# Optimization experiments

Measured on AMD Instinct MI355X. Metric: run time of the kernel, lower is better.

Reference implementation:

```python
import jax, jax.numpy as jnp
import numpy as np

B, T, H, NIN, D = 128, 64, 100, 3, 10


def _gru_cell(x, h, Wih, Whh, bih, bhh):
    # torch GRU cell: r,z,n gate ordering
    gi = x @ Wih.T + bih
    gh = h @ Whh.T + bhh
    ir, iz, inn = jnp.split(gi, 3, axis=-1)
    hr, hz, hn = jnp.split(gh, 3, axis=-1)
    r = jax.nn.sigmoid(ir + hr)
    z = jax.nn.sigmoid(iz + hz)
    n = jnp.tanh(inn + r * hn)
    return (1.0 - z) * n + z * h


def setup_inputs():
    keys = iter(jax.random.split(jax.random.key(0), 64))
    def rn(shape, scale):
        return jax.random.normal(next(keys), shape, dtype=jnp.float32) * scale
    inp = {"received": jax.random.normal(next(keys), (B, T, NIN), dtype=jnp.float32)}
    s = float(1.0 / np.sqrt(H))
    for p in ("w1", "w2"):
        inp[p + "_ih0"] = rn((3 * H, NIN), s)
        inp[p + "_hh0"] = rn((3 * H, H), s)
        inp[p + "_bih0"] = rn((3 * H,), s)
        inp[p + "_bhh0"] = rn((3 * H,), s)
        inp[p + "_ih1"] = rn((3 * H, H), s)
        inp[p + "_hh1"] = rn((3 * H, H), s)
        inp[p + "_bih1"] = rn((3 * H,), s)
        inp[p + "_bhh1"] = rn((3 * H,), s)
    s2 = float(1.0 / np.sqrt(2 * H))
    inp["attn_w"] = rn((1, 2 * H), s2)
    inp["attn_b"] = rn((1,), s2)
    inp["ctx_w"] = rn((H, 2 * H), s2)
    inp["ctx_b"] = rn((H,), s2)
    inp["out_w"] = rn((1, 2 * H), s2)
    inp["out_b"] = rn((1,), s2)
    return inp


def _forward(received, P1, P2, attn_w, attn_b, ctx_w, ctx_b, out_w, out_b):
    def two_layer(x, h, P):
        ih0, hh0, bih0, bhh0, ih1, hh1, bih1, bhh1 = P
        h0 = _gru_cell(x, h[0], ih0, hh0, bih0, bhh0)
        h1 = _gru_cell(h0, h[1], ih1, hh1, bih1, bhh1)
        # out = top-layer hidden; new hidden state [2,B,H]
        return h1, jnp.stack([h0, h1])

    def attend(hn, cache, t):
        # hn [2,B,H] (raw GRU hidden), cache [2,B,T,H] of past raw hiddens
        hrep = jnp.broadcast_to(hn[:, :, None, :], cache.shape)
        e = (jnp.concatenate([hrep, cache], axis=-1) @ attn_w.T)[..., 0] + attn_b[0]  # [2,B,T]
        mask = jnp.arange(T) < jnp.maximum(t, 1)  # safe mask (never all-False)
        a = jax.nn.softmax(jnp.where(mask, e, -1e30), axis=-1)
        c = jnp.einsum('lbt,lbth->lbh', a, cache)
        return jnp.concatenate([c, hn], axis=-1) @ ctx_w.T + ctx_b

    x_tm = jnp.transpose(received, (1, 0, 2))  # [T,B,NIN]
    h_init = jnp.zeros((2, B, H), jnp.float32)
    cache_init = jnp.zeros((2, B, T, H), jnp.float32)

    def step(carry, inp):
        h1, h2, c1, c2 = carry
        x, t = inp
        o1, h1n = two_layer(x, h1, P1)
        o2, h2n = two_layer(x, h2, P2)
        # attention over hiddens from steps 0..t-1 (cache updated AFTER attending)
        h1mix = attend(h1n, c1, t)
        h2mix = attend(h2n, c2, t)
        c1 = jax.lax.dynamic_update_slice(c1, h1n[:, :, None, :], (0, 0, t, 0))
        c2 = jax.lax.dynamic_update_slice(c2, h2n[:, :, None, :], (0, 0, t, 0))
        first = (t == 0)
        h1next = jnp.where(first, h1n, h1mix)
        h2next = jnp.where(first, h2n, h2mix)
        return (h1next, h2next, c1, c2), (o1, o2)

    _, (out1, out2) = jax.lax.scan(step, (h_init, h_init, cache_init, cache_init),
                                   (x_tm, jnp.arange(T)))
    out1 = jnp.transpose(out1, (1, 0, 2))  # [B,T,H]
    out2 = jnp.transpose(out2, (1, 0, 2))
    # readout: bit i pairs rnn_out1[i] with rnn_out2[min(i+D, T-1)]
    idx = jnp.minimum(jnp.arange(T) + D, T - 1)
    rnn_out = jnp.concatenate([out1, out2[:, idx, :]], axis=-1)  # [B,T,2H]
    logits = rnn_out @ out_w.T + out_b  # dec_act == 'linear'
    return jax.nn.sigmoid(logits)  # [B,T,1]


def reference(received, w1_ih0, w1_hh0, w1_bih0, w1_bhh0, w1_ih1, w1_hh1, w1_bih1, w1_bhh1,
              w2_ih0, w2_hh0, w2_bih0, w2_bhh0, w2_ih1, w2_hh1, w2_bih1, w2_bhh1,
              attn_w, attn_b, ctx_w, ctx_b, out_w, out_b):
    P1 = (w1_ih0, w1_hh0, w1_bih0, w1_bhh0, w1_ih1, w1_hh1, w1_bih1, w1_bhh1)
    P2 = (w2_ih0, w2_hh0, w2_bih0, w2_bhh0, w2_ih1, w2_hh1, w2_bih1, w2_bhh1)
    return _forward(received, P1, P2, attn_w, attn_b, ctx_w, ctx_b, out_w, out_b)
```

## Files before the change

### kernel.cpp

```cpp
#include <hip/hip_runtime.h>
#include <stdint.h>

#define H100 100
#define T64  64
#define NB   128
#define DLAG 10

#define OFF_HH0 0
#define OFF_IH1 30000
#define OFF_HH1 60000
#define OFF_CTX 90000
#define OFF_AWC 100000
#define OFF_OW  100050
#define OFF_P   100152

typedef _Float16 half2_t __attribute__((ext_vector_type(2)));
typedef __fp16   pk16x2  __attribute__((ext_vector_type(2)));

__device__ __forceinline__ float fdot2u(uint32_t a, uint32_t b, float c) {
#if __has_builtin(__builtin_amdgcn_fdot2)
    return __builtin_amdgcn_fdot2(__builtin_bit_cast(half2_t, a),
                                  __builtin_bit_cast(half2_t, b), c, false);
#else
    half2_t ha = __builtin_bit_cast(half2_t, a), hb = __builtin_bit_cast(half2_t, b);
    return c + (float)ha[0]*(float)hb[0] + (float)ha[1]*(float)hb[1];
#endif
}
__device__ __forceinline__ uint32_t pkrtz(float a, float b) {
    pk16x2 h = __builtin_amdgcn_cvt_pkrtz(a, b);
    return __builtin_bit_cast(uint32_t, h);
}
__device__ __forceinline__ uint32_t pk_rn(float a, float b) {
    half2_t h; h[0] = (_Float16)a; h[1] = (_Float16)b;
    return __builtin_bit_cast(uint32_t, h);
}
__device__ __forceinline__ float lo16(uint32_t u){ return (float)__builtin_bit_cast(half2_t,u)[0]; }
__device__ __forceinline__ float hi16(uint32_t u){ return (float)__builtin_bit_cast(half2_t,u)[1]; }
__device__ __forceinline__ float sigm(float x){ return 1.f/(1.f+__expf(-x)); }
__device__ __forceinline__ float tanhfast(float x){ return 1.f - 2.f/(1.f+__expf(2.f*x)); }
__device__ __forceinline__ float gru_el(float pr, float pz, float gin, float ghn, float hp) {
    float r = sigm(pr), z = sigm(pz);
    float n = tanhfast(gin + r*ghn);
    return (1.f - z)*n + z*hp;
}
__device__ __forceinline__ float wsum(float v){
    #pragma unroll
    for (int off = 32; off; off >>= 1) v += __shfl_xor(v, off);
    return v;
}
__device__ __forceinline__ float wmax(float v){
    #pragma unroll
    for (int off = 32; off; off >>= 1) v = fmaxf(v, __shfl_xor(v, off));
    return v;
}

struct SMem {
    alignas(16) uint32_t cache_t[2][50][66];
    alignas(16) float grz1[200];
    alignas(16) float gin1[104];
    alignas(16) float ghn1[104];
    alignas(16) float grz2[200];
    alignas(16) float gin2[104];
    alignas(16) float ghn2[104];
    alignas(16) float sv[2][64];
    alignas(16) float atile[2][64];
    alignas(16) uint32_t cpkq[2][52];
    alignas(16) uint32_t h0c[52];
    alignas(16) uint32_t h1c[52];
    alignas(16) uint32_t hn0[52];
    alignas(16) uint32_t hn1[52];
    alignas(16) float x[192];
};

__global__ void prep_pack(const float* __restrict__ w1hh0, const float* __restrict__ w2hh0,
                          const float* __restrict__ w1ih1, const float* __restrict__ w2ih1,
                          const float* __restrict__ w1hh1, const float* __restrict__ w2hh1,
                          const float* __restrict__ attw,  const float* __restrict__ ctxw,
                          const float* __restrict__ outw,  uint32_t* __restrict__ ws) {
    int g = blockIdx.x*blockDim.x + threadIdx.x;
    if (g < 30000) {
        int br = g/15000, idx = g%15000;
        int j = idx/50, kp = idx%50;
        const float* w = br ? w2hh0 : w1hh0;
        ws[OFF_HH0 + g] = pk_rn(w[j*H100+2*kp], w[j*H100+2*kp+1]);
    } else if (g < 60000) {
        int t2 = g-30000; int br = t2/15000, idx = t2%15000;
        int j = idx/50, kp = idx%50;
        const float* w = br ? w2ih1 : w1ih1;
        ws[OFF_IH1 + t2] = pk_rn(w[j*H100+2*kp], w[j*H100+2*kp+1]);
    } else if (g < 90000) {
        int t2 = g-60000; int br = t2/15000, idx = t2%15000;
        int j = idx/50, kp = idx%50;
        const float* w = br ? w2hh1 : w1hh1;
        ws[OFF_HH1 + t2] = pk_rn(w[j*H100+2*kp], w[j*H100+2*kp+1]);
    } else if (g < 100000) {
        int idx = g-90000; int o = idx/100, kp = idx%100;
        ws[OFF_CTX + idx] = pk_rn(ctxw[o*200+2*kp], ctxw[o*200+2*kp+1]);
    } else if (g < 100050) {
        int i2 = g-100000;
        ws[OFF_AWC + i2] = pk_rn(attw[100+2*i2], attw[101+2*i2]);
    } else if (g < 100150) {
        int t2 = g-100050; int br = t2/50, i2 = t2%50;
        ws[OFF_OW + t2] = pk_rn(outw[br*H100+2*i2], outw[br*H100+2*i2+1]);
    }
}

__global__ __launch_bounds__(512, 1)
void gru_seq(const float* __restrict__ recv,
             const float* __restrict__ ih0_1, const float* __restrict__ bih0_1,
             const float* __restrict__ bhh0_1, const float* __restrict__ bih1_1,
             const float* __restrict__ bhh1_1,
             const float* __restrict__ ih0_2, const float* __restrict__ bih0_2,
             const float* __restrict__ bhh0_2, const float* __restrict__ bih1_2,
             const float* __restrict__ bhh1_2,
             const float* __restrict__ ctxb,
             uint32_t* __restrict__ ws) {
    __shared__ SMem S;
    const int tid = threadIdx.x;
    const int w   = tid >> 6;
    const int la  = tid & 63;
    const int br  = blockIdx.x >> 7;
    const int b   = blockIdx.x & 127;

    const float* ih0 = br ? ih0_2  : ih0_1;
    const float* bi0 = br ? bih0_2 : bih0_1;
    const float* bh0 = br ? bhh0_2 : bhh0_1;
    const float* bi1 = br ? bih1_2 : bih1_1;
    const float* bh1 = br ? bhh1_2 : bhh1_1;

    for (int i = tid; i < 192; i += 512) S.x[i] = recv[b*192 + i];
    for (int i = tid; i < 2*50*66; i += 512) ((uint32_t*)S.cache_t)[i] = 0u;
    if (tid < 128) S.sv[tid>>6][tid&63] = 0.f;
    if (tid < 104) { S.cpkq[0][tid>>1] = 0u; S.cpkq[1][tid>>1] = 0u; }
    if (tid >= 128 && tid < 180) { int i2 = tid-128; S.h0c[i2]=0u; S.h1c[i2]=0u; S.hn0[i2]=0u; S.hn1[i2]=0u; }

    uint32_t wreg[150];
    float fb0=0.f, fb1=0.f, fb2=0.f, fb3=0.f;
    float rix0=0.f, rix1=0.f, rix2=0.f;
    int cl=0, co=0;
    if (tid < 300) {
        const uint32_t* p0 = ws + OFF_HH0 + br*15000 + tid*50;
        const uint32_t* p1 = ws + OFF_HH1 + br*15000 + tid*50;
        const uint32_t* p2 = ws + OFF_IH1 + br*15000 + tid*50;
        #pragma unroll
        for (int k = 0; k < 50; ++k) { wreg[k] = p0[k]; wreg[50+k] = p1[k]; wreg[100+k] = p2[k]; }
        fb0 = bi0[tid]; fb1 = bh0[tid]; fb2 = bi1[tid]; fb3 = bh1[tid];
        rix0 = ih0[tid*3]; rix1 = ih0[tid*3+1]; rix2 = ih0[tid*3+2];
    } else if (tid < 500) {
        const int idx = tid - 300;
        cl = (idx >= 100) ? 1 : 0;
        co = idx - cl*100;
        const uint32_t* pc = ws + OFF_CTX + co*100;
        #pragma unroll
        for (int k = 0; k < 100; ++k) wreg[k] = pc[k];
        fb0 = ctxb[co];
    }
    uint32_t rawc = 0u, rowp = 0u;
    if ((w == 5 || w == 6) && la < 50) rawc = ws[OFF_AWC + la];
    if (w == 7 && la < 50) rowp = ws[OFF_OW + br*50 + la];
    float* p_out = (float*)(ws + OFF_P);

    float gh1save = 0.f;
    __syncthreads();

    for (int t = 0; t < T64; ++t) {
        if (tid < 300) {
            float x0 = S.x[3*t], x1 = S.x[3*t+1], x2 = S.x[3*t+2];
            float accI = fb0 + rix0*x0 + rix1*x1 + rix2*x2;
            float a0=0.f,a1=0.f,a2=0.f,a3=0.f, b0=0.f,b1=0.f,b2=0.f,b3=0.f;
            #pragma unroll
            for (int i = 0; i < 12; ++i) {
                uint4 h0 = *(const uint4*)&S.h0c[4*i];
                uint4 h1 = *(const uint4*)&S.h1c[4*i];
                a0 = fdot2u(wreg[4*i],    h0.x, a0);
                b0 = fdot2u(wreg[50+4*i], h1.x, b0);
                a1 = fdot2u(wreg[4*i+1],    h0.y, a1);
                b1 = fdot2u(wreg[50+4*i+1], h1.y, b1);
                a2 = fdot2u(wreg[4*i+2],    h0.z, a2);
                b2 = fdot2u(wreg[50+4*i+2], h1.z, b2);
                a3 = fdot2u(wreg[4*i+3],    h0.w, a3);
                b3 = fdot2u(wreg[50+4*i+3], h1.w, b3);
            }
            {
                uint2 h0t = *(const uint2*)&S.h0c[48];
                uint2 h1t = *(const uint2*)&S.h1c[48];
                a0 = fdot2u(wreg[48],    h0t.x, a0);
                b0 = fdot2u(wreg[98],    h1t.x, b0);
                a1 = fdot2u(wreg[49],    h0t.y, a1);
                b1 = fdot2u(wreg[99],    h1t.y, b1);
            }
            float acc0 = fb1 + ((a0+a1)+(a2+a3));
            gh1save    = fb3 + ((b0+b1)+(b2+b3));
            if (tid < 200) S.grz1[tid] = accI + acc0;
            else { S.gin1[tid-200] = accI; S.ghn1[tid-200] = acc0; }
        } else if (w == 5 || w == 6) {
            const int l = w - 5;
            const int m = (t > 1) ? t : 1;
            float sval = S.sv[l][la];
            float sv2  = (la < m) ? sval : -3e38f;
            float mx   = wmax(sv2);
            float p    = (la < m) ? __expf(sv2 - mx) : 0.f;
            float ssum = wsum(p);
            S.atile[l][la] = p;
            if (la < 50) {
                float c0 = 0.f, c1 = 0.f;
                const uint32_t* crow = &S.cache_t[l][la][0];
                const int np = (m + 1) >> 1;
                for (int tb = 0; tb < np; tb += 8) {
                    float2 ap[8]; uint2 cp[8];
                    #pragma unroll
                    for (int j = 0; j < 8; ++j) {
                        ap[j] = *(const float2*)&S.atile[l][2*(tb+j)];
                        cp[j] = *(const uint2*)&crow[2*(tb+j)];
                    }
                    #pragma unroll
                    for (int j = 0; j < 8; ++j) {
                        c0 += ap[j].x*lo16(cp[j].x) + ap[j].y*lo16(cp[j].y);
                        c1 += ap[j].x*hi16(cp[j].x) + ap[j].y*hi16(cp[j].y);
                    }
                }
                float inv = 1.f/ssum;
                S.cpkq[l][la] = pkrtz(c0*inv, c1*inv);
            }
        }
        __syncthreads();
        if (w == 5) {
            uint32_t hn0p = 0u;
            if (la < 50) {
                float2 pr = *(const float2*)&S.grz1[2*la];
                float2 pz = *(const float2*)&S.grz1[100+2*la];
                float2 gi = *(const float2*)&S.gin1[2*la];
                float2 gh = *(const float2*)&S.ghn1[2*la];
                uint32_t hp = S.h0c[la];
                float h0 = gru_el(pr.x, pz.x, gi.x, gh.x, lo16(hp));
                float h1 = gru_el(pr.y, pz.y, gi.y, gh.y, hi16(hp));
                hn0p = pkrtz(h0, h1);
                S.hn0[la] = hn0p;
                S.cache_t[0][la][t] = hn0p;
            }
            float v = (la < 50) ? fdot2u(rawc, hn0p, 0.f) : 0.f;
            v = wsum(v);
            if (la == 0) S.sv[0][t] = v;
        } else if (w == 7 && t > 0) {
            float v = (la < 50) ? fdot2u(rowp, S.hn1[la], 0.f) : 0.f;
            v = wsum(v);
            if (la == 0) p_out[br*8192 + b*64 + (t-1)] = v;
        }
        __syncthreads();
        if (tid < 300) {
            float g0=0.f,g1=0.f,g2=0.f,g3=0.f;
            #pragma unroll
            for (int i = 0; i < 12; ++i) {
                uint4 h = *(const uint4*)&S.hn0[4*i];
                g0 = fdot2u(wreg[100+4*i],   h.x, g0);
                g1 = fdot2u(wreg[100+4*i+1], h.y, g1);
                g2 = fdot2u(wreg[100+4*i+2], h.z, g2);
                g3 = fdot2u(wreg[100+4*i+3], h.w, g3);
            }
            {
                uint2 ht = *(const uint2*)&S.hn0[48];
                g0 = fdot2u(wreg[148], ht.x, g0);
                g1 = fdot2u(wreg[149], ht.y, g1);
            }
            float gi1 = fb2 + ((g0+g1)+(g2+g3));
            if (tid < 200) S.grz2[tid] = gi1 + gh1save;
            else { S.gin2[tid-200] = gi1; S.ghn2[tid-200] = gh1save; }
        }
        __syncthreads();
        if (w == 6) {
            uint32_t hn1p = 0u;
            if (la < 50) {
                float2 pr = *(const float2*)&S.grz2[2*la];
                float2 pz = *(const float2*)&S.grz2[100+2*la];
                float2 gi = *(const float2*)&S.gin2[2*la];
                float2 gh = *(const float2*)&S.ghn2[2*la];
                uint32_t hp = S.h1c[la];
                float h0 = gru_el(pr.x, pz.x, gi.x, gh.x, lo16(hp));
                float h1 = gru_el(pr.y, pz.y, gi.y, gh.y, hi16(hp));
                hn1p = pkrtz(h0, h1);
                S.hn1[la] = hn1p;
                S.cache_t[1][la][t] = hn1p;
            }
            float v = (la < 50) ? fdot2u(rawc, hn1p, 0.f) : 0.f;
            v = wsum(v);
            if (la == 0) S.sv[1][t] = v;
        }
        __syncthreads();
        if (tid >= 300 && tid < 500) {
            const uint32_t* cparr = S.cpkq[cl];
            const uint32_t* hnarr = cl ? S.hn1 : S.hn0;
            float p0=fb0, p1=0.f, p2=0.f, p3=0.f;
            float q0=0.f, q1=0.f, q2=0.f, q3=0.f;
            #pragma unroll
            for (int i = 0; i < 12; ++i) {
                uint4 c = *(const uint4*)&cparr[4*i];
                uint4 h = *(const uint4*)&hnarr[4*i];
                p0 = fdot2u(wreg[4*i],   c.x, p0);
                q0 = fdot2u(wreg[50+4*i],   h.x, q0);
                p1 = fdot2u(wreg[4*i+1], c.y, p1);
                q1 = fdot2u(wreg[50+4*i+1], h.y, q1);
                p2 = fdot2u(wreg[4*i+2], c.z, p2);
                q2 = fdot2u(wreg[50+4*i+2], h.z, q2);
                p3 = fdot2u(wreg[4*i+3], c.w, p3);
                q3 = fdot2u(wreg[50+4*i+3], h.w, q3);
            }
            {
                uint2 c = *(const uint2*)&cparr[48];
                uint2 h = *(const uint2*)&hnarr[48];
                p0 = fdot2u(wreg[48], c.x, p0);
                q0 = fdot2u(wreg[98], h.x, q0);
                p1 = fdot2u(wreg[49], c.y, p1);
                q1 = fdot2u(wreg[99], h.y, q1);
            }
            float m0 = ((p0+p1)+(p2+p3)) + ((q0+q1)+(q2+q3));
            float n0 = __shfl_down(m0, 1);
            if (!(co & 1)) {
                uint32_t packed = (t == 0) ? hnarr[co>>1] : pkrtz(m0, n0);
                if (cl) S.h1c[co>>1] = packed; else S.h0c[co>>1] = packed;
            }
        }
        __syncthreads();
    }
    if (w == 7) {
        float v = (la < 50) ? fdot2u(rowp, S.hn1[la], 0.f) : 0.f;
        v = wsum(v);
        if (la == 0) p_out[br*8192 + b*64 + 63] = v;
    }
}

__global__ void fin_out(const uint32_t* __restrict__ ws, const float* __restrict__ outb,
                        float* __restrict__ out) {
    int i = blockIdx.x*blockDim.x + threadIdx.x;
    if (i >= NB*T64) return;
    int b = i >> 6, t = i & 63;
    const float* p = (const float*)(ws + OFF_P);
    int t2 = t + DLAG; if (t2 > T64-1) t2 = T64-1;
    float logit = p[0*8192 + b*64 + t] + p[1*8192 + b*64 + t2] + outb[0];
    out[i] = 1.f/(1.f+__expf(-logit));
}

extern "C" void kernel_launch(void* const* d_in, const int* in_sizes, int n_in,
                              void* d_out, int out_size, void* d_ws, size_t ws_size,
                              hipStream_t stream) {
    const float* recv   = (const float*)d_in[0];
    const float* w1ih0  = (const float*)d_in[1];
    const float* w1hh0  = (const float*)d_in[2];
    const float* w1bih0 = (const float*)d_in[3];
    const float* w1bhh0 = (const float*)d_in[4];
    const float* w1ih1  = (const float*)d_in[5];
    const float* w1hh1  = (const float*)d_in[6];
    const float* w1bih1 = (const float*)d_in[7];
    const float* w1bhh1 = (const float*)d_in[8];
    const float* w2ih0  = (const float*)d_in[9];
    const float* w2hh0  = (const float*)d_in[10];
    const float* w2bih0 = (const float*)d_in[11];
    const float* w2bhh0 = (const float*)d_in[12];
    const float* w2ih1  = (const float*)d_in[13];
    const float* w2hh1  = (const float*)d_in[14];
    const float* w2bih1 = (const float*)d_in[15];
    const float* w2bhh1 = (const float*)d_in[16];
    const float* attw   = (const float*)d_in[17];
    const float* ctxw   = (const float*)d_in[19];
    const float* ctxb   = (const float*)d_in[20];
    const float* outw   = (const float*)d_in[21];
    const float* outb   = (const float*)d_in[22];
    uint32_t* ws = (uint32_t*)d_ws;
    float* out = (float*)d_out;

    prep_pack<<<(100150 + 255)/256, 256, 0, stream>>>(
        w1hh0, w2hh0, w1ih1, w2ih1, w1hh1, w2hh1, attw, ctxw, outw, ws);

    gru_seq<<<256, 512, 0, stream>>>(
        recv,
        w1ih0, w1bih0, w1bhh0, w1bih1, w1bhh1,
        w2ih0, w2bih0, w2bhh0, w2bih1, w2bhh1,
        ctxb, ws);

    fin_out<<<(NB*T64 + 255)/256, 256, 0, stream>>>(ws, outb, out);
}
```

Measured before the change: 227.1 us.

## Split ctx matvec across 400 threads and move layer-1 hh matvec to phase two

The context projection is now split in half along K across 400 threads (tid 100..499), each holding 50 packed weights in a separate register array; the halves are combined with a lane shuffle. The layer-1 recurrent matvec (h1c · W_hh1) moves from the first phase into the second phase, which otherwise only runs the small GRU elementwise warps. The aim is to shorten the critical path of phases one and three so the serial per-timestep barrier chain gets shorter. The cost is extra registers in threads that hold both wreg and creg (tid 100..299), which may hurt occupancy or cause spills.

```diff
diff --git a/kernel.cpp b/kernel.cpp
--- a/kernel.cpp
+++ b/kernel.cpp
@@ -135,9 +135,10 @@
     if (tid >= 128 && tid < 180) { int i2 = tid-128; S.h0c[i2]=0u; S.h1c[i2]=0u; S.hn0[i2]=0u; S.hn1[i2]=0u; }
 
     uint32_t wreg[150];
-    float fb0=0.f, fb1=0.f, fb2=0.f, fb3=0.f;
+    uint32_t creg[50];
+    float fb0=0.f, fb1=0.f, fb2=0.f, fb3=0.f, fcb=0.f;
     float rix0=0.f, rix1=0.f, rix2=0.f;
-    int cl=0, co=0;
+    int kh=0, cl=0, co=0;
     if (tid < 300) {
         const uint32_t* p0 = ws + OFF_HH0 + br*15000 + tid*50;
         const uint32_t* p1 = ws + OFF_HH1 + br*15000 + tid*50;
@@ -146,14 +147,16 @@
         for (int k = 0; k < 50; ++k) { wreg[k] = p0[k]; wreg[50+k] = p1[k]; wreg[100+k] = p2[k]; }
         fb0 = bi0[tid]; fb1 = bh0[tid]; fb2 = bi1[tid]; fb3 = bh1[tid];
         rix0 = ih0[tid*3]; rix1 = ih0[tid*3+1]; rix2 = ih0[tid*3+2];
-    } else if (tid < 500) {
-        const int idx = tid - 300;
-        cl = (idx >= 100) ? 1 : 0;
-        co = idx - cl*100;
-        const uint32_t* pc = ws + OFF_CTX + co*100;
+    }
+    if (tid >= 100 && tid < 500) {
+        const int j = (tid - 100) >> 1;
+        kh = tid & 1;
+        cl = (j >= 100) ? 1 : 0;
+        co = j - cl*100;
+        const uint32_t* pc = ws + OFF_CTX + co*100 + kh*50;
         #pragma unroll
-        for (int k = 0; k < 100; ++k) wreg[k] = pc[k];
-        fb0 = ctxb[co];
+        for (int k = 0; k < 50; ++k) creg[k] = pc[k];
+        fcb = kh ? 0.f : ctxb[co];
     }
     uint32_t rawc = 0u, rowp = 0u;
     if ((w == 5 || w == 6) && la < 50) rawc = ws[OFF_AWC + la];
@@ -167,30 +170,21 @@
         if (tid < 300) {
             float x0 = S.x[3*t], x1 = S.x[3*t+1], x2 = S.x[3*t+2];
             float accI = fb0 + rix0*x0 + rix1*x1 + rix2*x2;
-            float a0=0.f,a1=0.f,a2=0.f,a3=0.f, b0=0.f,b1=0.f,b2=0.f,b3=0.f;
+            float a0=0.f,a1=0.f,a2=0.f,a3=0.f;
             #pragma unroll
             for (int i = 0; i < 12; ++i) {
                 uint4 h0 = *(const uint4*)&S.h0c[4*i];
-                uint4 h1 = *(const uint4*)&S.h1c[4*i];
-                a0 = fdot2u(wreg[4*i],    h0.x, a0);
-                b0 = fdot2u(wreg[50+4*i], h1.x, b0);
-                a1 = fdot2u(wreg[4*i+1],    h0.y, a1);
-                b1 = fdot2u(wreg[50+4*i+1], h1.y, b1);
-                a2 = fdot2u(wreg[4*i+2],    h0.z, a2);
-                b2 = fdot2u(wreg[50+4*i+2], h1.z, b2);
-                a3 = fdot2u(wreg[4*i+3],    h0.w, a3);
-                b3 = fdot2u(wreg[50+4*i+3], h1.w, b3);
+                a0 = fdot2u(wreg[4*i],   h0.x, a0);
+                a1 = fdot2u(wreg[4*i+1], h0.y, a1);
+                a2 = fdot2u(wreg[4*i+2], h0.z, a2);
+                a3 = fdot2u(wreg[4*i+3], h0.w, a3);
             }
             {
                 uint2 h0t = *(const uint2*)&S.h0c[48];
-                uint2 h1t = *(const uint2*)&S.h1c[48];
-                a0 = fdot2u(wreg[48],    h0t.x, a0);
-                b0 = fdot2u(wreg[98],    h1t.x, b0);
-                a1 = fdot2u(wreg[49],    h0t.y, a1);
-                b1 = fdot2u(wreg[99],    h1t.y, b1);
+                a0 = fdot2u(wreg[48], h0t.x, a0);
+                a1 = fdot2u(wreg[49], h0t.y, a1);
             }
             float acc0 = fb1 + ((a0+a1)+(a2+a3));
-            gh1save    = fb3 + ((b0+b1)+(b2+b3));
             if (tid < 200) S.grz1[tid] = accI + acc0;
             else { S.gin1[tid-200] = accI; S.ghn1[tid-200] = acc0; }
         } else if (w == 5 || w == 6) {
@@ -224,7 +218,23 @@
             }
         }
         __syncthreads();
-        if (w == 5) {
+        if (tid < 300) {
+            float b0=0.f,b1=0.f,b2=0.f,b3=0.f;
+            #pragma unroll
+            for (int i = 0; i < 12; ++i) {
+                uint4 h1 = *(const uint4*)&S.h1c[4*i];
+                b0 = fdot2u(wreg[50+4*i],   h1.x, b0);
+                b1 = fdot2u(wreg[50+4*i+1], h1.y, b1);
+                b2 = fdot2u(wreg[50+4*i+2], h1.z, b2);
+                b3 = fdot2u(wreg[50+4*i+3], h1.w, b3);
+            }
+            {
+                uint2 h1t = *(const uint2*)&S.h1c[48];
+                b0 = fdot2u(wreg[98], h1t.x, b0);
+                b1 = fdot2u(wreg[99], h1t.y, b1);
+            }
+            gh1save = fb3 + ((b0+b1)+(b2+b3));
+        } else if (w == 5) {
             uint32_t hn0p = 0u;
             if (la < 50) {
                 float2 pr = *(const float2*)&S.grz1[2*la];
@@ -286,36 +296,28 @@
             if (la == 0) S.sv[1][t] = v;
         }
         __syncthreads();
-        if (tid >= 300 && tid < 500) {
-            const uint32_t* cparr = S.cpkq[cl];
-            const uint32_t* hnarr = cl ? S.hn1 : S.hn0;
-            float p0=fb0, p1=0.f, p2=0.f, p3=0.f;
-            float q0=0.f, q1=0.f, q2=0.f, q3=0.f;
+        if (tid >= 100 && tid < 500) {
+            const uint32_t* oparr = kh ? (cl ? S.hn1 : S.hn0) : S.cpkq[cl];
+            float p0=fcb, p1=0.f, p2=0.f, p3=0.f;
             #pragma unroll
             for (int i = 0; i < 12; ++i) {
-                uint4 c = *(const uint4*)&cparr[4*i];
-                uint4 h = *(const uint4*)&hnarr[4*i];
-                p0 = fdot2u(wreg[4*i],   c.x, p0);
-                q0 = fdot2u(wreg[50+4*i],   h.x, q0);
-                p1 = fdot2u(wreg[4*i+1], c.y, p1);
-                q1 = fdot2u(wreg[50+4*i+1], h.y, q1);
-                p2 = fdot2u(wreg[4*i+2], c.z, p2);
-                q2 = fdot2u(wreg[50+4*i+2], h.z, q2);
-                p3 = fdot2u(wreg[4*i+3], c.w, p3);
-                q3 = fdot2u(wreg[50+4*i+3], h.w, q3);
+                uint4 c = *(const uint4*)&oparr[4*i];
+                p0 = fdot2u(creg[4*i],   c.x, p0);
+                p1 = fdot2u(creg[4*i+1], c.y, p1);
+                p2 = fdot2u(creg[4*i+2], c.z, p2);
+                p3 = fdot2u(creg[4*i+3], c.w, p3);
             }
             {
-                uint2 c = *(const uint2*)&cparr[48];
-                uint2 h = *(const uint2*)&hnarr[48];
-                p0 = fdot2u(wreg[48], c.x, p0);
-                q0 = fdot2u(wreg[98], h.x, q0);
-                p1 = fdot2u(wreg[49], c.y, p1);
-                q1 = fdot2u(wreg[99], h.y, q1);
-            }
-            float m0 = ((p0+p1)+(p2+p3)) + ((q0+q1)+(q2+q3));
-            float n0 = __shfl_down(m0, 1);
-            if (!(co & 1)) {
-                uint32_t packed = (t == 0) ? hnarr[co>>1] : pkrtz(m0, n0);
+                uint2 c = *(const uint2*)&oparr[48];
+                p0 = fdot2u(creg[48], c.x, p0);
+                p1 = fdot2u(creg[49], c.y, p1);
+            }
+            float half = (p0+p1) + (p2+p3);
+            float full = half + __shfl_down(half, 1);
+            float nxt = __shfl_down(full, 2);
+            if (kh == 0 && !(co & 1)) {
+                const uint32_t* hnarr = cl ? S.hn1 : S.hn0;
+                uint32_t packed = (t == 0) ? hnarr[co>>1] : pkrtz(full, nxt);
                 if (cl) S.h1c[co>>1] = packed; else S.h0c[co>>1] = packed;
             }
         }
```

Measured after the change: 230.8 us. No clear change (+1.6%).
